# Kernel optimization log

Hardware: AMD Instinct MI355X
Metric: run time of the kernel (lower is better)

The kernel has to match this reference:

```python
import jax, jax.numpy as jnp
import numpy as np

B, T, N = 16, 1024, 512

def setup_inputs() -> dict:
    key = jax.random.key(0)
    ks = jax.random.split(key, 6)
    scale = 1.0 / np.sqrt(N)
    x = jax.random.normal(ks[0], (B, T, N), dtype=jnp.float32)
    Wq = jax.random.normal(ks[1], (N, N), dtype=jnp.float32) * scale
    Wk = jax.random.normal(ks[2], (N, N), dtype=jnp.float32) * scale
    Wv = jax.random.normal(ks[3], (N, N), dtype=jnp.float32) * scale
    Wp = jax.random.normal(ks[4], (N, N), dtype=jnp.float32) * scale
    bp = jnp.zeros((N,), dtype=jnp.float32)
    return {"x": x, "Wq": Wq, "Wk": Wk, "Wv": Wv, "Wp": Wp, "bp": bp}

def reference(x, Wq, Wk, Wv, Wp, bp):
    # x: [B, T, N]; conv1d(k=1) over node channels == 'oi,bit->bot' on x^T [B,N,T]
    xt = jnp.swapaxes(x, -1, -2)                     # [B, N, T]
    q = jnp.einsum('oi,bit->bot', Wq, xt)            # [B, N, T]
    k = jnp.einsum('oi,bit->bot', Wk, xt)
    v = jnp.einsum('oi,bit->bot', Wv, xt)
    n = x.shape[-1]
    attn = jnp.einsum('bnt,bmt->bnm', q, k) * (n ** -0.5)  # [B, N, N]
    attn = jax.nn.softmax(attn, axis=-1)
    px = jnp.einsum('bnm,bmt->bnt', attn, v)         # [B, N, T]
    px = jnp.swapaxes(px, -1, -2)                    # [B, T, N]
    out = jnp.einsum('btn,on->bto', px, Wp) + bp     # Linear(N,N)
    return out
```

## Files before the change

### kernel.cpp

```cpp
#include <hip/hip_runtime.h>
#include <stdint.h>

#define BB 16
#define TT 1024
#define NN 512

typedef unsigned short u16;
typedef __bf16 bf16_t;
typedef bf16_t bf16x8 __attribute__((ext_vector_type(8)));
typedef float f32x4 __attribute__((ext_vector_type(4)));

struct alignas(8) U16x4 { u16 x, y, z, w; };
struct alignas(16) F32x4 { float x, y, z, w; };

__device__ __forceinline__ u16 f2bf(float f) {
    union { float f; uint32_t u; } v; v.f = f;
    uint32_t r = v.u + 0x7fffu + ((v.u >> 16) & 1u);
    return (u16)(r >> 16);
}

__device__ __forceinline__ void gload_lds16(const void* g, void* l) {
    __builtin_amdgcn_global_load_lds(
        (const __attribute__((address_space(1))) void*)g,
        (__attribute__((address_space(3))) void*)l, 16, 0, 0);
}

__global__ __launch_bounds__(256)
void cvt_f32_bf16(const float* __restrict__ in, u16* __restrict__ out, int n4) {
    int i = blockIdx.x * blockDim.x + threadIdx.x;
    int stride = gridDim.x * blockDim.x;
    for (int c = i; c < n4; c += stride) {
        F32x4 f = ((const F32x4*)in)[c];
        U16x4 u;
        u.x = f2bf(f.x); u.y = f2bf(f.y); u.z = f2bf(f.z); u.w = f2bf(f.w);
        ((U16x4*)out)[c] = u;
    }
}

__global__ __launch_bounds__(256)
void cvt_weights(const float* __restrict__ Wq, const float* __restrict__ Wk,
                 const float* __restrict__ Wv, const float* __restrict__ Wp,
                 u16* __restrict__ out) {
    const int c = blockIdx.x * 256 + threadIdx.x;
    const int w = c >> 16;
    const int idx = c & 65535;
    const float* src = (w == 0) ? Wq : (w == 1) ? Wk : (w == 2) ? Wv : Wp;
    F32x4 f = ((const F32x4*)src)[idx];
    U16x4 u;
    u.x = f2bf(f.x); u.y = f2bf(f.y); u.z = f2bf(f.z); u.w = f2bf(f.w);
    ((U16x4*)out)[c] = u;
}

template<int MODE>
__global__ __launch_bounds__(256)
void gemm_nt(const u16* __restrict__ Ag, const u16* __restrict__ Bg,
             void* __restrict__ Cg, const float* __restrict__ bias,
             int M, int Nc, int K, int lda, int ldb,
             long sA, long sB, long sC)
{
    const u16* A  = Ag + (long)blockIdx.z * sA;
    const u16* Bt = Bg + (long)blockIdx.z * sB;

    __shared__ u16 As[8192];
    __shared__ u16 Bs[8192];

    const int tid  = threadIdx.x;
    const int wave = tid >> 6;
    const int lane = tid & 63;
    const int arow0 = blockIdx.y * 128;
    const int brow0 = blockIdx.x * 128;
    const int wr = (wave >> 1) * 64;
    const int wc = (wave & 1) * 64;

    f32x4 zero = {0.f, 0.f, 0.f, 0.f};
    f32x4 acc[4][4];
#pragma unroll
    for (int i = 0; i < 4; i++)
#pragma unroll
        for (int j = 0; j < 4; j++) acc[i][j] = zero;

    const int kTiles = K >> 6;
    for (int kt = 0; kt < kTiles; ++kt) {
#pragma unroll
        for (int it = 0; it < 4; ++it) {
            const int off  = it * 4096 + wave * 1024 + lane * 16;
            const int row  = off >> 7;
            const int kb   = off & 127;
            const int gcol = kb ^ ((row & 7) << 4);
            gload_lds16((const char*)A  + ((long)(arow0 + row) * lda + kt * 64) * 2 + gcol,
                        (char*)As + it * 4096 + wave * 1024);
            gload_lds16((const char*)Bt + ((long)(brow0 + row) * ldb + kt * 64) * 2 + gcol,
                        (char*)Bs + it * 4096 + wave * 1024);
        }
        __syncthreads();

#pragma unroll
        for (int kk = 0; kk < 2; ++kk) {
            bf16x8 av[4], bv[4];
            const int kbyte = kk * 64 + ((lane >> 4) << 4);
#pragma unroll
            for (int m = 0; m < 4; m++) {
                const int row = wr + m * 16 + (lane & 15);
                av[m] = *(const bf16x8*)((const char*)As + row * 128 + (kbyte ^ ((row & 7) << 4)));
            }
#pragma unroll
            for (int n = 0; n < 4; n++) {
                const int row = wc + n * 16 + (lane & 15);
                bv[n] = *(const bf16x8*)((const char*)Bs + row * 128 + (kbyte ^ ((row & 7) << 4)));
            }
#pragma unroll
            for (int m = 0; m < 4; m++)
#pragma unroll
                for (int n = 0; n < 4; n++)
                    acc[m][n] = __builtin_amdgcn_mfma_f32_16x16x32_bf16(av[m], bv[n], acc[m][n], 0, 0, 0);
        }
        __syncthreads();
    }

    const int r0 = (lane >> 4) << 2;
    const int cl = lane & 15;
#pragma unroll
    for (int m = 0; m < 4; m++) {
        const long gm = (long)arow0 + wr + m * 16 + r0;
#pragma unroll
        for (int n = 0; n < 4; n++) {
            const long gn = (long)brow0 + wc + n * 16 + cl;
            if (MODE == 0) {
                u16* O = (u16*)Cg + blockIdx.z * sC;
#pragma unroll
                for (int r = 0; r < 4; r++)
                    O[(gm + r) * Nc + gn] = f2bf(acc[m][n][r]);
            } else if (MODE == 4) {
                const long b = gm >> 10;
                const long t = gm & 1023;
                if (gn < 1024) {
                    u16* O = (u16*)Cg + (gn >> 9) * ((long)BB * NN * TT);
                    const long col = gn & 511;
                    U16x4 u;
                    u.x = f2bf(acc[m][n][0]); u.y = f2bf(acc[m][n][1]);
                    u.z = f2bf(acc[m][n][2]); u.w = f2bf(acc[m][n][3]);
                    *(U16x4*)(O + (b * 512 + col) * 1024 + t) = u;
                } else {
                    u16* V = (u16*)Cg + 2L * BB * NN * TT;
                    const int vc = (int)gn - 1024;
#pragma unroll
                    for (int r = 0; r < 4; r++)
                        V[(gm + r) * NN + vc] = f2bf(acc[m][n][r]);
                }
            } else {
                float* O = (float*)Cg + blockIdx.z * sC;
                const float bb = (MODE == 3) ? bias[gn] : 0.f;
#pragma unroll
                for (int r = 0; r < 4; r++)
                    O[(gm + r) * Nc + gn] = acc[m][n][r] + bb;
            }
        }
    }
}

__global__ __launch_bounds__(256)
void softmax_rows(float* __restrict__ S)
{
    const long r = blockIdx.x;
    float* row = S + r * 512;
    const int t = threadIdx.x;
    const int lane = t & 63, wave = t >> 6;
    const float scale = 0.04419417382415922f;

    float a = row[t] * scale;
    float b = row[t + 256] * scale;

    float m = fmaxf(a, b);
#pragma unroll
    for (int o = 32; o; o >>= 1) m = fmaxf(m, __shfl_xor(m, o, 64));

    __shared__ float red[8];
    if (lane == 0) red[wave] = m;
    __syncthreads();
    m = fmaxf(fmaxf(red[0], red[1]), fmaxf(red[2], red[3]));

    float e0 = __expf(a - m), e1 = __expf(b - m);
    float s = e0 + e1;
#pragma unroll
    for (int o = 32; o; o >>= 1) s += __shfl_xor(s, o, 64);
    if (lane == 0) red[wave + 4] = s;
    __syncthreads();
    s = red[4] + red[5] + red[6] + red[7];
    const float inv = 1.f / s;

    u16* P = (u16*)row;
    P[t]       = f2bf(e0 * inv);
    P[t + 256] = f2bf(e1 * inv);
}

extern "C" void kernel_launch(void* const* d_in, const int* in_sizes, int n_in,
                              void* d_out, int out_size, void* d_ws, size_t ws_size,
                              hipStream_t stream)
{
    (void)in_sizes; (void)n_in; (void)out_size; (void)ws_size;
    const float* x  = (const float*)d_in[0];
    const float* Wq = (const float*)d_in[1];
    const float* Wk = (const float*)d_in[2];
    const float* Wv = (const float*)d_in[3];
    const float* Wp = (const float*)d_in[4];
    const float* bp = (const float*)d_in[5];
    float* out = (float*)d_out;

    char* ws = (char*)d_ws;
    size_t o = 0;
    auto alloc = [&](size_t bytes) {
        char* p = ws + o;
        o = (o + bytes + 255) & ~(size_t)255;
        return p;
    };
    u16* xb  = (u16*)alloc((size_t)BB * TT * NN * 2);
    u16* wb  = (u16*)alloc((size_t)4 * NN * NN * 2);
    u16* qkv = (u16*)alloc((size_t)3 * BB * NN * TT * 2);
    float* S = (float*)alloc((size_t)BB * NN * NN * 4);
    u16* px  = xb;

    const u16* qb  = qkv;
    const u16* kbp = qkv + (size_t)BB * NN * TT;
    const u16* vb  = qkv + (size_t)2 * BB * NN * TT;
    const u16* wpb = wb + (size_t)3 * NN * NN;

    cvt_f32_bf16<<<dim3(2048), dim3(256), 0, stream>>>(x, xb, (BB * TT * NN) / 4);
    cvt_weights<<<dim3(1024), dim3(256), 0, stream>>>(Wq, Wk, Wv, Wp, wb);

    const dim3 blk(256);

    const dim3 gq(12, 128, 1);
    gemm_nt<4><<<gq, blk, 0, stream>>>(xb, wb, qkv, nullptr,
                                       BB * TT, 1536, NN, NN, NN, 0, 0, 0);

    const dim3 g2(NN / 128, NN / 128, BB);
    gemm_nt<2><<<g2, blk, 0, stream>>>(qb, kbp, S, nullptr, NN, NN, TT, TT, TT,
                                       (long)NN * TT, (long)NN * TT, (long)NN * NN);

    softmax_rows<<<dim3(BB * NN), dim3(256), 0, stream>>>(S);

    const dim3 g3(NN / 128, TT / 128, BB);
    gemm_nt<0><<<g3, blk, 0, stream>>>(vb, (const u16*)S, px, nullptr, TT, NN, NN, NN, 1024,
                                       (long)TT * NN, (long)NN * 1024, (long)TT * NN);

    const dim3 g1(NN / 128, (BB * TT) / 128, 1);
    gemm_nt<3><<<g1, blk, 0, stream>>>(px, wpb, out, bp, BB * TT, NN, NN, NN, NN, 0, 0, 0);
}
```

Baseline: 205.6 us.

## Split-K the QK^T GEMM and add XCD-aware block swizzling

The per-batch Q·K^T GEMM had only 256 workgroups, so it now runs as split-K over two halves of T, giving 512 workgroups. Each half writes fp32 partials into a doubled S buffer, and the softmax kernel adds the two partials before scaling. All GEMMs also remap block IDs so that neighbouring tiles run on the same XCD, which should improve L2 reuse. The cost is an extra 16 MB fp32 partial buffer that must be written and then read back by softmax.

```diff
diff --git a/kernel.cpp b/kernel.cpp
--- a/kernel.cpp
+++ b/kernel.cpp
@@ -23,6 +23,16 @@
     __builtin_amdgcn_global_load_lds(
         (const __attribute__((address_space(1))) void*)g,
         (__attribute__((address_space(3))) void*)l, 16, 0, 0);
+}
+
+__device__ __forceinline__ void xcd_swizzle(int gx, int gy, int& bx, int& by) {
+    const int nwg  = gx * gy;
+    const int orig = by * gx + bx;
+    const int q = nwg >> 3, r = nwg & 7;
+    const int xcd = orig & 7, loc = orig >> 3;
+    const int swz = (xcd < r ? xcd * (q + 1) : r * (q + 1) + (xcd - r) * q) + loc;
+    bx = swz % gx;
+    by = swz / gx;
 }
 
 __global__ __launch_bounds__(256)
@@ -51,24 +61,29 @@
     ((U16x4*)out)[c] = u;
 }
 
-template<int MODE>
+template<int MODE, int SPLITK>
 __global__ __launch_bounds__(256)
 void gemm_nt(const u16* __restrict__ Ag, const u16* __restrict__ Bg,
              void* __restrict__ Cg, const float* __restrict__ bias,
              int M, int Nc, int K, int lda, int ldb,
              long sA, long sB, long sC)
 {
-    const u16* A  = Ag + (long)blockIdx.z * sA;
-    const u16* Bt = Bg + (long)blockIdx.z * sB;
+    int zb = blockIdx.z, kof = 0;
+    if (SPLITK) { kof = (zb >> 4) * K; zb &= 15; }
+    const u16* A  = Ag + (long)zb * sA + kof;
+    const u16* Bt = Bg + (long)zb * sB + kof;
 
     __shared__ u16 As[8192];
     __shared__ u16 Bs[8192];
+
+    int bx = blockIdx.x, by = blockIdx.y;
+    xcd_swizzle(gridDim.x, gridDim.y, bx, by);
 
     const int tid  = threadIdx.x;
     const int wave = tid >> 6;
     const int lane = tid & 63;
-    const int arow0 = blockIdx.y * 128;
-    const int brow0 = blockIdx.x * 128;
+    const int arow0 = by * 128;
+    const int brow0 = bx * 128;
     const int wr = (wave >> 1) * 64;
     const int wc = (wave & 1) * 64;
 
@@ -159,16 +174,17 @@
 }
 
 __global__ __launch_bounds__(256)
-void softmax_rows(float* __restrict__ S)
+void softmax_rows(float* __restrict__ S0, const float* __restrict__ S1)
 {
     const long r = blockIdx.x;
-    float* row = S + r * 512;
+    float* row0 = S0 + r * 512;
+    const float* row1 = S1 + r * 512;
     const int t = threadIdx.x;
     const int lane = t & 63, wave = t >> 6;
     const float scale = 0.04419417382415922f;
 
-    float a = row[t] * scale;
-    float b = row[t + 256] * scale;
+    float a = (row0[t]       + row1[t])       * scale;
+    float b = (row0[t + 256] + row1[t + 256]) * scale;
 
     float m = fmaxf(a, b);
 #pragma unroll
@@ -188,7 +204,7 @@
     s = red[4] + red[5] + red[6] + red[7];
     const float inv = 1.f / s;
 
-    u16* P = (u16*)row;
+    u16* P = (u16*)row0;
     P[t]       = f2bf(e0 * inv);
     P[t + 256] = f2bf(e1 * inv);
 }
@@ -216,13 +232,14 @@
     u16* xb  = (u16*)alloc((size_t)BB * TT * NN * 2);
     u16* wb  = (u16*)alloc((size_t)4 * NN * NN * 2);
     u16* qkv = (u16*)alloc((size_t)3 * BB * NN * TT * 2);
-    float* S = (float*)alloc((size_t)BB * NN * NN * 4);
+    float* S = (float*)alloc((size_t)2 * BB * NN * NN * 4);
     u16* px  = xb;
 
     const u16* qb  = qkv;
     const u16* kbp = qkv + (size_t)BB * NN * TT;
     const u16* vb  = qkv + (size_t)2 * BB * NN * TT;
     const u16* wpb = wb + (size_t)3 * NN * NN;
+    float* S1 = S + (size_t)BB * NN * NN;
 
     cvt_f32_bf16<<<dim3(2048), dim3(256), 0, stream>>>(x, xb, (BB * TT * NN) / 4);
     cvt_weights<<<dim3(1024), dim3(256), 0, stream>>>(Wq, Wk, Wv, Wp, wb);
@@ -230,19 +247,19 @@
     const dim3 blk(256);
 
     const dim3 gq(12, 128, 1);
-    gemm_nt<4><<<gq, blk, 0, stream>>>(xb, wb, qkv, nullptr,
-                                       BB * TT, 1536, NN, NN, NN, 0, 0, 0);
-
-    const dim3 g2(NN / 128, NN / 128, BB);
-    gemm_nt<2><<<g2, blk, 0, stream>>>(qb, kbp, S, nullptr, NN, NN, TT, TT, TT,
-                                       (long)NN * TT, (long)NN * TT, (long)NN * NN);
-
-    softmax_rows<<<dim3(BB * NN), dim3(256), 0, stream>>>(S);
+    gemm_nt<4, 0><<<gq, blk, 0, stream>>>(xb, wb, qkv, nullptr,
+                                          BB * TT, 1536, NN, NN, NN, 0, 0, 0);
+
+    const dim3 g2(NN / 128, NN / 128, 2 * BB);
+    gemm_nt<2, 1><<<g2, blk, 0, stream>>>(qb, kbp, S, nullptr, NN, NN, TT / 2, TT, TT,
+                                          (long)NN * TT, (long)NN * TT, (long)NN * NN);
+
+    softmax_rows<<<dim3(BB * NN), dim3(256), 0, stream>>>(S, S1);
 
     const dim3 g3(NN / 128, TT / 128, BB);
-    gemm_nt<0><<<g3, blk, 0, stream>>>(vb, (const u16*)S, px, nullptr, TT, NN, NN, NN, 1024,
-                                       (long)TT * NN, (long)NN * 1024, (long)TT * NN);
+    gemm_nt<0, 0><<<g3, blk, 0, stream>>>(vb, (const u16*)S, px, nullptr, TT, NN, NN, NN, 1024,
+                                          (long)TT * NN, (long)NN * 1024, (long)TT * NN);
 
     const dim3 g1(NN / 128, (BB * TT) / 128, 1);
-    gemm_nt<3><<<g1, blk, 0, stream>>>(px, wpb, out, bp, BB * TT, NN, NN, NN, NN, 0, 0, 0);
-}
+    gemm_nt<3, 0><<<g1, blk, 0, stream>>>(px, wpb, out, bp, BB * TT, NN, NN, NN, NN, 0, 0, 0);
+}
```

Result: faster. 189.9 us (-7.6%).
